# Performance work log

Hardware: AMD Instinct MI355X
Metric: run time of the kernel (lower is better)

## Reference

```python
import jax, jax.numpy as jnp
import numpy as np

N_NODES = 50000
N_EDGES = 800000
IN_FEATS = 256
HEADS = 4
OUT_FEATS = 32
NEG_SLOPE = 0.2


def setup_inputs() -> dict:
    key = jax.random.key(0)
    ks = jax.random.split(key, 8)
    return {
        "feat": jax.random.normal(ks[0], (N_NODES, IN_FEATS), dtype=jnp.float32),
        "edge_weight": jax.random.uniform(ks[1], (N_EDGES,), dtype=jnp.float32),
        "src": jax.random.randint(ks[2], (N_EDGES,), 0, N_NODES, dtype=jnp.int32),
        "dst": jax.random.randint(ks[3], (N_EDGES,), 0, N_NODES, dtype=jnp.int32),
        "W_fc": jax.random.normal(ks[4], (HEADS * OUT_FEATS, IN_FEATS), dtype=jnp.float32) * 0.05,
        "W_edge": jax.random.normal(ks[5], (HEADS * OUT_FEATS, 1), dtype=jnp.float32) * 0.05,
        "attn_l": jax.random.normal(ks[6], (1, HEADS, OUT_FEATS), dtype=jnp.float32) * 0.1,
        "attn_r": jax.random.normal(ks[7], (1, HEADS, OUT_FEATS), dtype=jnp.float32) * 0.1,
        "bias": jnp.zeros((HEADS * OUT_FEATS,), dtype=jnp.float32),
    }


def reference(feat, edge_weight, src, dst, W_fc, W_edge, attn_l, attn_r, bias):
    N = feat.shape[0]
    H, F = attn_l.shape[1], attn_l.shape[2]
    # node projection: [N, H, F]
    feat_hf = (feat @ W_fc.T).reshape(N, H, F)
    el = jnp.sum(feat_hf * attn_l, axis=-1)  # [N, H]
    er = jnp.sum(feat_hf * attn_r, axis=-1)  # [N, H]
    # edgefc(weight.unsqueeze(-1)): Linear(1, H*F) -> weight[e] * W_edge[:,0]
    edge_ft = (edge_weight[:, None] * W_edge[:, 0][None, :]).reshape(-1, H, F)  # [E,H,F]
    # e = leaky_relu(u_add_v(el, er) + edge_ft); broadcast [E,H,1] + [E,H,F]
    e = (el[src] + er[dst])[:, :, None] + edge_ft
    e = jnp.where(e >= 0, e, NEG_SLOPE * e)
    # edge softmax per destination (elementwise over H, F)
    m = jax.ops.segment_max(e, dst, num_segments=N)  # [N,H,F]
    m = jnp.where(jnp.isfinite(m), m, 0.0)
    ex = jnp.exp(e - m[dst])
    s = jax.ops.segment_sum(ex, dst, num_segments=N)  # [N,H,F]
    a = ex / s[dst]
    # weighted aggregation: sum_{e: dst=v} ft[src[e]] * a[e]
    rst = jax.ops.segment_sum(feat_hf[src] * a, dst, num_segments=N)  # [N,H,F]
    rst = rst + bias.reshape(1, H, F)
    return rst
```

## Files before the change

kernel.cpp:

```cpp
#include <hip/hip_runtime.h>

#define NN 50000
#define NE 800000
#define KF 256
#define HF 128
#define NEG 0.2f
#define INVLN2 1.44269504088896340736f

#define NB 391
#define EB 391
#define EPB 2048
#define PREP_BLOCKS 64
#define PROJ_BLOCKS 782

typedef __attribute__((ext_vector_type(8))) short bf16x8;
typedef __attribute__((ext_vector_type(4))) float f32x4;

static __device__ __forceinline__ unsigned bf16_rne(float x) {
  unsigned u = __float_as_uint(x);
  return (u + 0x7fffu + ((u >> 16) & 1u)) >> 16;
}
static __device__ __forceinline__ unsigned cvt_pk(float lo, float hi) {
  unsigned r;
  asm("v_cvt_pk_bf16_f32 %0, %1, %2" : "=v"(r) : "v"(lo), "v"(hi));
  return r;
}
static __device__ __forceinline__ float exp2_raw(float x) {
  float r;
  asm("v_exp_f32 %0, %1" : "=v"(r) : "v"(x));
  return r;
}

__global__ __launch_bounds__(256) void k1_prep_hist(
    const float* __restrict__ Wfc, unsigned* __restrict__ wfcb,
    const int* __restrict__ dst, int* __restrict__ histT) {
  if (blockIdx.x < PREP_BLOCKS) {
    int t = blockIdx.x * 256 + threadIdx.x;
    int e2 = t & 3;
    int l  = (t >> 2) & 63;
    int ct = (t >> 8) & 7;
    int ks = t >> 11;
    int j = ct * 16 + (l & 15);
    int k = ks * 32 + (l >> 4) * 8 + 2 * e2;
    unsigned lo = bf16_rne(Wfc[j * KF + k]);
    unsigned hi = bf16_rne(Wfc[j * KF + k + 1]);
    wfcb[t] = lo | (hi << 16);
    return;
  }
  int e = blockIdx.x - PREP_BLOCKS;
  __shared__ int hist[NB];
  for (int b = threadIdx.x; b < NB; b += 256) hist[b] = 0;
  __syncthreads();
  int base = e * EPB;
  int cnt = min(EPB, NE - base);
  for (int k = threadIdx.x; k < cnt; k += 256) {
    int d = dst[base + k];
    atomicAdd(&hist[d >> 7], 1);
  }
  __syncthreads();
  for (int b = threadIdx.x; b < NB; b += 256) histT[b * EB + e] = hist[b];
}

__global__ __launch_bounds__(256) void k2_proj_scan(
    const float* __restrict__ feat, const unsigned* __restrict__ wfcb,
    unsigned* __restrict__ ftp, const int* __restrict__ histT,
    int* __restrict__ colbase, int* __restrict__ bucketTotal,
    const float* __restrict__ al, const float* __restrict__ ar,
    float* __restrict__ el, float* __restrict__ er) {
  if (blockIdx.x >= PROJ_BLOCKS) {
    int b = blockIdx.x - PROJ_BLOCKS;
    __shared__ int buf[512];
    int t = threadIdx.x;
    int a0 = (t < EB) ? histT[b * EB + t] : 0;
    int a1 = (t + 256 < EB) ? histT[b * EB + t + 256] : 0;
    buf[t] = a0;
    buf[t + 256] = a1;
    __syncthreads();
    for (int o = 1; o < 512; o <<= 1) {
      int x0 = (t >= o) ? buf[t - o] : 0;
      int x1 = buf[t + 256 - o];
      __syncthreads();
      buf[t] += x0;
      buf[t + 256] += x1;
      __syncthreads();
    }
    if (t < EB) colbase[t * NB + b] = buf[t] - a0;
    if (t + 256 < EB) colbase[(t + 256) * NB + b] = buf[t + 256] - a1;
    if (t == 0) bucketTotal[b] = buf[EB - 1];
    return;
  }
  int wid = (blockIdx.x * 256 + threadIdx.x) >> 6;
  if (wid >= NN / 16) return;
  const int lane = threadIdx.x & 63;
  const int m0 = wid * 16;
  const int row = m0 + (lane & 15);
  const int kb = (lane >> 4) * 8;

  f32x4 acc[8];
#pragma unroll
  for (int ct = 0; ct < 8; ct++) acc[ct] = (f32x4){0.f, 0.f, 0.f, 0.f};

  const float4* a4p = (const float4*)(feat + row * KF + kb);
#pragma unroll
  for (int ks = 0; ks < 8; ks++) {
    float4 a0 = a4p[ks * 8];
    float4 a1 = a4p[ks * 8 + 1];
    union { int4 i; bf16x8 s; } ua;
    ua.i = make_int4((int)cvt_pk(a0.x, a0.y), (int)cvt_pk(a0.z, a0.w),
                     (int)cvt_pk(a1.x, a1.y), (int)cvt_pk(a1.z, a1.w));
    bf16x8 af = ua.s;
#pragma unroll
    for (int ct = 0; ct < 8; ct++) {
      union { int4 i; bf16x8 s; } ub;
      ub.i = *(const int4*)&wfcb[((ks * 8 + ct) * 64 + lane) * 4];
      acc[ct] = __builtin_amdgcn_mfma_f32_16x16x32_bf16(af, ub.s, acc[ct], 0, 0, 0);
    }
  }

  const int rbase = m0 + (lane >> 4) * 4;
  const int l15 = lane & 15;
  float alv0[4], alv1[4], arv0[4], arv1[4];
#pragma unroll
  for (int t2 = 0; t2 < 4; t2++) {
    alv0[t2] = al[t2 * 32 + l15];
    alv1[t2] = al[t2 * 32 + 16 + l15];
    arv0[t2] = ar[t2 * 32 + l15];
    arv1[t2] = ar[t2 * 32 + 16 + l15];
  }
  float pl_[4][4], pr_[4][4];
#pragma unroll
  for (int ct2 = 0; ct2 < 4; ct2++) {
#pragma unroll
    for (int r = 0; r < 4; r++) {
      unsigned wv = cvt_pk(acc[2 * ct2][r], acc[2 * ct2 + 1][r]);
      ftp[(rbase + r) * 64 + ct2 * 16 + l15] = wv;
      float f0 = __uint_as_float(wv << 16);
      float f1 = __uint_as_float(wv & 0xffff0000u);
      pl_[r][ct2] = f0 * alv0[ct2] + f1 * alv1[ct2];
      pr_[r][ct2] = f0 * arv0[ct2] + f1 * arv1[ct2];
    }
  }
#pragma unroll
  for (int o = 1; o < 16; o <<= 1) {
#pragma unroll
    for (int r = 0; r < 4; r++) {
#pragma unroll
      for (int hh = 0; hh < 4; hh++) {
        pl_[r][hh] += __shfl_xor(pl_[r][hh], o, 64);
        pr_[r][hh] += __shfl_xor(pr_[r][hh], o, 64);
      }
    }
  }
  if (l15 == 0) {
#pragma unroll
    for (int r = 0; r < 4; r++) {
#pragma unroll
      for (int hh = 0; hh < 4; hh++) {
        el[(rbase + r) * 4 + hh] = pl_[r][hh] * INVLN2;
        er[(rbase + r) * 4 + hh] = pr_[r][hh] * INVLN2;
      }
    }
  }
}

__global__ __launch_bounds__(256) void k4_scatter(
    const int* __restrict__ dst, const int* __restrict__ src,
    const float* __restrict__ ew, const int* __restrict__ colbase,
    const int* __restrict__ bucketTotal, int* __restrict__ bucketBase,
    int2* __restrict__ tmp) {
  __shared__ int buf[512];
  __shared__ int sbase[NB];
  __shared__ int lcnt[NB];
  int t = threadIdx.x;
  int e = blockIdx.x;
  int a0 = (t < NB) ? bucketTotal[t] : 0;
  int a1 = (t + 256 < NB) ? bucketTotal[t + 256] : 0;
  buf[t] = a0;
  buf[t + 256] = a1;
  for (int b = t; b < NB; b += 256) lcnt[b] = 0;
  __syncthreads();
  for (int o = 1; o < 512; o <<= 1) {
    int x0 = (t >= o) ? buf[t - o] : 0;
    int x1 = buf[t + 256 - o];
    __syncthreads();
    buf[t] += x0;
    buf[t + 256] += x1;
    __syncthreads();
  }
  if (t < NB) {
    int bb0 = buf[t] - a0;
    sbase[t] = bb0 + colbase[e * NB + t];
    if (e == 0) bucketBase[t] = bb0;
  }
  if (t + 256 < NB) {
    int bb1 = buf[t + 256] - a1;
    sbase[t + 256] = bb1 + colbase[e * NB + t + 256];
    if (e == 0) bucketBase[t + 256] = bb1;
  }
  if (e == 0 && t == 0) bucketBase[NB] = buf[NB - 1];
  __syncthreads();
  int base = e * EPB;
  int cnt = min(EPB, NE - base);
  for (int k = t; k < cnt; k += 256) {
    int i = base + k;
    int d = dst[i];
    unsigned s = (unsigned)src[i];
    float w = ew[i];
    int r = atomicAdd(&lcnt[d >> 7], 1);
    int pos = sbase[d >> 7] + r;
    tmp[pos] = make_int2((int)(s | ((unsigned)d << 16)), __float_as_int(w));
  }
}

__global__ __launch_bounds__(256) void k5_bucket(
    const int2* __restrict__ tmp, const int* __restrict__ bucketBase,
    int* __restrict__ segbeg, int* __restrict__ segend, int2* __restrict__ es8) {
  int b = blockIdx.x;
  int ebase = bucketBase[b], eend = bucketBase[b + 1];
  int vbase = b * 128;
  __shared__ int cnt[128], buf[128], cur[128];
  int t = threadIdx.x;
  if (t < 128) cnt[t] = 0;
  __syncthreads();
  for (int i = ebase + t; i < eend; i += 256) {
    unsigned x = (unsigned)tmp[i].x;
    atomicAdd(&cnt[(x >> 16) & 127], 1);
  }
  __syncthreads();
  if (t < 128) buf[t] = cnt[t];
  __syncthreads();
  for (int o = 1; o < 128; o <<= 1) {
    int x = (t < 128 && t >= o) ? buf[t - o] : 0;
    __syncthreads();
    if (t < 128) buf[t] += x;
    __syncthreads();
  }
  if (t < 128) {
    cur[t] = buf[t] - cnt[t];
    int v = vbase + t;
    if (v < NN) {
      segbeg[v] = ebase + cur[t];
      segend[v] = ebase + buf[t];
    }
  }
  __syncthreads();
  for (int i = ebase + t; i < eend; i += 256) {
    int2 rec = tmp[i];
    unsigned x = (unsigned)rec.x;
    int r = atomicAdd(&cur[(x >> 16) & 127], 1);
    es8[ebase + r] = make_int2((int)(x & 0xFFFFu), rec.y);
  }
}

__global__ __launch_bounds__(256) void agg_kernel(
    const unsigned* __restrict__ ftp, const float* __restrict__ el,
    const float* __restrict__ er, const int2* __restrict__ es8,
    const int* __restrict__ segbeg, const int* __restrict__ segend,
    const float* __restrict__ We, const float* __restrict__ bias,
    float* __restrict__ out) {
  int wid = (blockIdx.x * blockDim.x + threadIdx.x) >> 6;
  if (wid >= NN) return;
  const int lane = threadIdx.x & 63;
  const int v = wid;
  int beg = __builtin_amdgcn_readfirstlane(segbeg[v]);
  int end = __builtin_amdgcn_readfirstlane(segend[v]);
  const int h = lane >> 4;
  const int c0 = h * 32 + (lane & 15), c1 = c0 + 16;
  const float wx = We[c0] * INVLN2, wy = We[c1] * INVLN2;
  const float bx = bias[c0], by = bias[c1];
  if (beg == end) {
    out[v * HF + c0] = bx;
    out[v * HF + c1] = by;
    return;
  }
  const float erv = er[v * 4 + h];
  float num0 = 0.f, num1 = 0.f, den0 = 0.f, den1 = 0.f;

#define EDGE(w_, u_, e_)                                            \
  {                                                                 \
    float base = (e_) + erv;                                        \
    float t0 = fmaf((w_), wx, base); t0 = fmaxf(t0, NEG * t0);      \
    float t1 = fmaf((w_), wy, base); t1 = fmaxf(t1, NEG * t1);      \
    float x0 = exp2_raw(t0), x1 = exp2_raw(t1);                     \
    float f0 = __uint_as_float((u_) << 16);                         \
    float f1 = __uint_as_float((u_) & 0xffff0000u);                 \
    num0 = fmaf(f0, x0, num0); den0 += x0;                          \
    num1 = fmaf(f1, x1, num1); den1 += x1;                          \
  }

  int i = beg;
  for (; i + 8 <= end; i += 8) {
    int2 q0 = es8[i],     q1 = es8[i + 1], q2 = es8[i + 2], q3 = es8[i + 3];
    int2 q4 = es8[i + 4], q5 = es8[i + 5], q6 = es8[i + 6], q7 = es8[i + 7];
    int s0 = __builtin_amdgcn_readfirstlane(q0.x);
    int s1 = __builtin_amdgcn_readfirstlane(q1.x);
    int s2 = __builtin_amdgcn_readfirstlane(q2.x);
    int s3 = __builtin_amdgcn_readfirstlane(q3.x);
    int s4 = __builtin_amdgcn_readfirstlane(q4.x);
    int s5 = __builtin_amdgcn_readfirstlane(q5.x);
    int s6 = __builtin_amdgcn_readfirstlane(q6.x);
    int s7 = __builtin_amdgcn_readfirstlane(q7.x);
    unsigned u0 = ftp[s0 * 64 + lane], u1 = ftp[s1 * 64 + lane];
    unsigned u2 = ftp[s2 * 64 + lane], u3 = ftp[s3 * 64 + lane];
    unsigned u4 = ftp[s4 * 64 + lane], u5 = ftp[s5 * 64 + lane];
    unsigned u6 = ftp[s6 * 64 + lane], u7 = ftp[s7 * 64 + lane];
    float e0 = el[s0 * 4 + h], e1 = el[s1 * 4 + h];
    float e2 = el[s2 * 4 + h], e3 = el[s3 * 4 + h];
    float e4 = el[s4 * 4 + h], e5 = el[s5 * 4 + h];
    float e6 = el[s6 * 4 + h], e7 = el[s7 * 4 + h];
    float w0 = __uint_as_float(__builtin_amdgcn_readfirstlane(q0.y));
    float w1 = __uint_as_float(__builtin_amdgcn_readfirstlane(q1.y));
    float w2 = __uint_as_float(__builtin_amdgcn_readfirstlane(q2.y));
    float w3 = __uint_as_float(__builtin_amdgcn_readfirstlane(q3.y));
    float w4 = __uint_as_float(__builtin_amdgcn_readfirstlane(q4.y));
    float w5 = __uint_as_float(__builtin_amdgcn_readfirstlane(q5.y));
    float w6 = __uint_as_float(__builtin_amdgcn_readfirstlane(q6.y));
    float w7 = __uint_as_float(__builtin_amdgcn_readfirstlane(q7.y));
    EDGE(w0, u0, e0); EDGE(w1, u1, e1); EDGE(w2, u2, e2); EDGE(w3, u3, e3);
    EDGE(w4, u4, e4); EDGE(w5, u5, e5); EDGE(w6, u6, e6); EDGE(w7, u7, e7);
  }
  for (; i < end; i++) {
    int2 q = es8[i];
    int s = __builtin_amdgcn_readfirstlane(q.x);
    unsigned u = ftp[s * 64 + lane];
    float ee = el[s * 4 + h];
    float w = __uint_as_float(__builtin_amdgcn_readfirstlane(q.y));
    EDGE(w, u, ee);
  }
#undef EDGE

  out[v * HF + c0] = num0 / den0 + bx;
  out[v * HF + c1] = num1 / den1 + by;
}

extern "C" void kernel_launch(void* const* d_in, const int* in_sizes, int n_in,
                              void* d_out, int out_size, void* d_ws, size_t ws_size,
                              hipStream_t stream) {
  const float* feat = (const float*)d_in[0];
  const float* ew   = (const float*)d_in[1];
  const int*   src  = (const int*)d_in[2];
  const int*   dst  = (const int*)d_in[3];
  const float* Wfc  = (const float*)d_in[4];
  const float* We   = (const float*)d_in[5];
  const float* al   = (const float*)d_in[6];
  const float* ar   = (const float*)d_in[7];
  const float* bias = (const float*)d_in[8];
  float* out = (float*)d_out;

  char* ws = (char*)d_ws;
  unsigned* ftp        = (unsigned*)(ws + 0);
  float* el            = (float*)(ws + 12800000);
  float* er            = (float*)(ws + 13600000);
  int* segbeg          = (int*)(ws + 14400000);
  int* segend          = (int*)(ws + 14600000);
  int2* es8            = (int2*)(ws + 14800000);
  int2* tmp            = (int2*)(ws + 21200000);
  int* histT           = (int*)(ws + 27600000);
  int* colbase         = (int*)(ws + 28211524);
  int* bucketTotal     = (int*)(ws + 28823048);
  int* bucketBase      = (int*)(ws + 28824612);
  unsigned* wfcb       = (unsigned*)(ws + 28826180);

  k1_prep_hist<<<PREP_BLOCKS + EB, 256, 0, stream>>>(Wfc, wfcb, dst, histT);
  k2_proj_scan<<<PROJ_BLOCKS + NB, 256, 0, stream>>>(feat, wfcb, ftp, histT, colbase,
                                                     bucketTotal, al, ar, el, er);
  k4_scatter<<<EB, 256, 0, stream>>>(dst, src, ew, colbase, bucketTotal, bucketBase,
                                     tmp);
  k5_bucket<<<NB, 256, 0, stream>>>(tmp, bucketBase, segbeg, segend, es8);
  agg_kernel<<<(NN * 64) / 256, 256, 0, stream>>>(ftp, el, er, es8, segbeg, segend, We,
                                                  bias, out);
}
```

Before: 91.40 us.

## Split node projection across scatter and bucket kernels to overlap latency-bound stages

The MFMA node-projection work is moved out of the scan kernel and split in two halves. Each half is appended as extra blocks to the scatter and bucket-sort kernels. The aim is to let compute-heavy GEMM blocks run alongside the small, atomic-bound histogram and scatter phases, which leave the GPU underused. The scan kernel becomes a standalone lightweight launch. The risk is that the larger proj blocks delay the critical-path scatter blocks, or that register and shared-memory pressure from the fused kernels lowers occupancy.

```diff
diff --git a/kernel.cpp b/kernel.cpp
--- a/kernel.cpp
+++ b/kernel.cpp
@@ -11,7 +11,8 @@
 #define EB 391
 #define EPB 2048
 #define PREP_BLOCKS 64
-#define PROJ_BLOCKS 782
+#define PROJ_WAVES 3125
+#define PH 391
 
 typedef __attribute__((ext_vector_type(8))) short bf16x8;
 typedef __attribute__((ext_vector_type(4))) float f32x4;
@@ -29,6 +30,83 @@
   float r;
   asm("v_exp_f32 %0, %1" : "=v"(r) : "v"(x));
   return r;
+}
+
+static __device__ __forceinline__ void proj_wave(
+    const float* __restrict__ feat, const unsigned* __restrict__ wfcb,
+    unsigned* __restrict__ ftp, const float* __restrict__ al,
+    const float* __restrict__ ar, float* __restrict__ el, float* __restrict__ er,
+    int wid, int lane) {
+  if (wid >= PROJ_WAVES) return;
+  const int m0 = wid * 16;
+  const int row = m0 + (lane & 15);
+  const int kb = (lane >> 4) * 8;
+
+  f32x4 acc[8];
+#pragma unroll
+  for (int ct = 0; ct < 8; ct++) acc[ct] = (f32x4){0.f, 0.f, 0.f, 0.f};
+
+  const float4* a4p = (const float4*)(feat + row * KF + kb);
+#pragma unroll
+  for (int ks = 0; ks < 8; ks++) {
+    float4 a0 = a4p[ks * 8];
+    float4 a1 = a4p[ks * 8 + 1];
+    union { int4 i; bf16x8 s; } ua;
+    ua.i = make_int4((int)cvt_pk(a0.x, a0.y), (int)cvt_pk(a0.z, a0.w),
+                     (int)cvt_pk(a1.x, a1.y), (int)cvt_pk(a1.z, a1.w));
+    bf16x8 af = ua.s;
+#pragma unroll
+    for (int ct = 0; ct < 8; ct++) {
+      union { int4 i; bf16x8 s; } ub;
+      ub.i = *(const int4*)&wfcb[((ks * 8 + ct) * 64 + lane) * 4];
+      acc[ct] = __builtin_amdgcn_mfma_f32_16x16x32_bf16(af, ub.s, acc[ct], 0, 0, 0);
+    }
+  }
+
+  const int rbase = m0 + (lane >> 4) * 4;
+  const int l15 = lane & 15;
+  float alv0[4], alv1[4], arv0[4], arv1[4];
+#pragma unroll
+  for (int t2 = 0; t2 < 4; t2++) {
+    alv0[t2] = al[t2 * 32 + l15];
+    alv1[t2] = al[t2 * 32 + 16 + l15];
+    arv0[t2] = ar[t2 * 32 + l15];
+    arv1[t2] = ar[t2 * 32 + 16 + l15];
+  }
+  float pl_[4][4], pr_[4][4];
+#pragma unroll
+  for (int ct2 = 0; ct2 < 4; ct2++) {
+#pragma unroll
+    for (int r = 0; r < 4; r++) {
+      unsigned wv = cvt_pk(acc[2 * ct2][r], acc[2 * ct2 + 1][r]);
+      ftp[(rbase + r) * 64 + ct2 * 16 + l15] = wv;
+      float f0 = __uint_as_float(wv << 16);
+      float f1 = __uint_as_float(wv & 0xffff0000u);
+      pl_[r][ct2] = f0 * alv0[ct2] + f1 * alv1[ct2];
+      pr_[r][ct2] = f0 * arv0[ct2] + f1 * arv1[ct2];
+    }
+  }
+#pragma unroll
+  for (int o = 1; o < 16; o <<= 1) {
+#pragma unroll
+    for (int r = 0; r < 4; r++) {
+#pragma unroll
+      for (int hh = 0; hh < 4; hh++) {
+        pl_[r][hh] += __shfl_xor(pl_[r][hh], o, 64);
+        pr_[r][hh] += __shfl_xor(pr_[r][hh], o, 64);
+      }
+    }
+  }
+  if (l15 == 0) {
+#pragma unroll
+    for (int r = 0; r < 4; r++) {
+#pragma unroll
+      for (int hh = 0; hh < 4; hh++) {
+        el[(rbase + r) * 4 + hh] = pl_[r][hh] * INVLN2;
+        er[(rbase + r) * 4 + hh] = pr_[r][hh] * INVLN2;
+      }
+    }
+  }
 }
 
 __global__ __launch_bounds__(256) void k1_prep_hist(
@@ -61,113 +139,44 @@
   for (int b = threadIdx.x; b < NB; b += 256) histT[b * EB + e] = hist[b];
 }
 
-__global__ __launch_bounds__(256) void k2_proj_scan(
-    const float* __restrict__ feat, const unsigned* __restrict__ wfcb,
-    unsigned* __restrict__ ftp, const int* __restrict__ histT,
-    int* __restrict__ colbase, int* __restrict__ bucketTotal,
-    const float* __restrict__ al, const float* __restrict__ ar,
-    float* __restrict__ el, float* __restrict__ er) {
-  if (blockIdx.x >= PROJ_BLOCKS) {
-    int b = blockIdx.x - PROJ_BLOCKS;
-    __shared__ int buf[512];
-    int t = threadIdx.x;
-    int a0 = (t < EB) ? histT[b * EB + t] : 0;
-    int a1 = (t + 256 < EB) ? histT[b * EB + t + 256] : 0;
-    buf[t] = a0;
-    buf[t + 256] = a1;
-    __syncthreads();
-    for (int o = 1; o < 512; o <<= 1) {
-      int x0 = (t >= o) ? buf[t - o] : 0;
-      int x1 = buf[t + 256 - o];
-      __syncthreads();
-      buf[t] += x0;
-      buf[t + 256] += x1;
-      __syncthreads();
-    }
-    if (t < EB) colbase[t * NB + b] = buf[t] - a0;
-    if (t + 256 < EB) colbase[(t + 256) * NB + b] = buf[t + 256] - a1;
-    if (t == 0) bucketTotal[b] = buf[EB - 1];
-    return;
-  }
-  int wid = (blockIdx.x * 256 + threadIdx.x) >> 6;
-  if (wid >= NN / 16) return;
-  const int lane = threadIdx.x & 63;
-  const int m0 = wid * 16;
-  const int row = m0 + (lane & 15);
-  const int kb = (lane >> 4) * 8;
-
-  f32x4 acc[8];
-#pragma unroll
-  for (int ct = 0; ct < 8; ct++) acc[ct] = (f32x4){0.f, 0.f, 0.f, 0.f};
-
-  const float4* a4p = (const float4*)(feat + row * KF + kb);
-#pragma unroll
-  for (int ks = 0; ks < 8; ks++) {
-    float4 a0 = a4p[ks * 8];
-    float4 a1 = a4p[ks * 8 + 1];
-    union { int4 i; bf16x8 s; } ua;
-    ua.i = make_int4((int)cvt_pk(a0.x, a0.y), (int)cvt_pk(a0.z, a0.w),
-                     (int)cvt_pk(a1.x, a1.y), (int)cvt_pk(a1.z, a1.w));
-    bf16x8 af = ua.s;
-#pragma unroll
-    for (int ct = 0; ct < 8; ct++) {
-      union { int4 i; bf16x8 s; } ub;
-      ub.i = *(const int4*)&wfcb[((ks * 8 + ct) * 64 + lane) * 4];
-      acc[ct] = __builtin_amdgcn_mfma_f32_16x16x32_bf16(af, ub.s, acc[ct], 0, 0, 0);
-    }
-  }
-
-  const int rbase = m0 + (lane >> 4) * 4;
-  const int l15 = lane & 15;
-  float alv0[4], alv1[4], arv0[4], arv1[4];
-#pragma unroll
-  for (int t2 = 0; t2 < 4; t2++) {
-    alv0[t2] = al[t2 * 32 + l15];
-    alv1[t2] = al[t2 * 32 + 16 + l15];
-    arv0[t2] = ar[t2 * 32 + l15];
-    arv1[t2] = ar[t2 * 32 + 16 + l15];
-  }
-  float pl_[4][4], pr_[4][4];
-#pragma unroll
-  for (int ct2 = 0; ct2 < 4; ct2++) {
-#pragma unroll
-    for (int r = 0; r < 4; r++) {
-      unsigned wv = cvt_pk(acc[2 * ct2][r], acc[2 * ct2 + 1][r]);
-      ftp[(rbase + r) * 64 + ct2 * 16 + l15] = wv;
-      float f0 = __uint_as_float(wv << 16);
-      float f1 = __uint_as_float(wv & 0xffff0000u);
-      pl_[r][ct2] = f0 * alv0[ct2] + f1 * alv1[ct2];
-      pr_[r][ct2] = f0 * arv0[ct2] + f1 * arv1[ct2];
-    }
-  }
-#pragma unroll
-  for (int o = 1; o < 16; o <<= 1) {
-#pragma unroll
-    for (int r = 0; r < 4; r++) {
-#pragma unroll
-      for (int hh = 0; hh < 4; hh++) {
-        pl_[r][hh] += __shfl_xor(pl_[r][hh], o, 64);
-        pr_[r][hh] += __shfl_xor(pr_[r][hh], o, 64);
-      }
-    }
-  }
-  if (l15 == 0) {
-#pragma unroll
-    for (int r = 0; r < 4; r++) {
-#pragma unroll
-      for (int hh = 0; hh < 4; hh++) {
-        el[(rbase + r) * 4 + hh] = pl_[r][hh] * INVLN2;
-        er[(rbase + r) * 4 + hh] = pr_[r][hh] * INVLN2;
-      }
-    }
-  }
-}
-
-__global__ __launch_bounds__(256) void k4_scatter(
+__global__ __launch_bounds__(256) void k2_scan(
+    const int* __restrict__ histT, int* __restrict__ colbase,
+    int* __restrict__ bucketTotal) {
+  int b = blockIdx.x;
+  __shared__ int buf[512];
+  int t = threadIdx.x;
+  int a0 = (t < EB) ? histT[b * EB + t] : 0;
+  int a1 = (t + 256 < EB) ? histT[b * EB + t + 256] : 0;
+  buf[t] = a0;
+  buf[t + 256] = a1;
+  __syncthreads();
+  for (int o = 1; o < 512; o <<= 1) {
+    int x0 = (t >= o) ? buf[t - o] : 0;
+    int x1 = buf[t + 256 - o];
+    __syncthreads();
+    buf[t] += x0;
+    buf[t + 256] += x1;
+    __syncthreads();
+  }
+  if (t < EB) colbase[t * NB + b] = buf[t] - a0;
+  if (t + 256 < EB) colbase[(t + 256) * NB + b] = buf[t + 256] - a1;
+  if (t == 0) bucketTotal[b] = buf[EB - 1];
+}
+
+__global__ __launch_bounds__(256) void k4_scatter_proj(
     const int* __restrict__ dst, const int* __restrict__ src,
     const float* __restrict__ ew, const int* __restrict__ colbase,
     const int* __restrict__ bucketTotal, int* __restrict__ bucketBase,
-    int2* __restrict__ tmp) {
+    int2* __restrict__ tmp,
+    const float* __restrict__ feat, const unsigned* __restrict__ wfcb,
+    unsigned* __restrict__ ftp, const float* __restrict__ al,
+    const float* __restrict__ ar, float* __restrict__ el, float* __restrict__ er) {
+  if (blockIdx.x >= EB) {
+    int pidx = blockIdx.x - EB;
+    proj_wave(feat, wfcb, ftp, al, ar, el, er,
+              (pidx * 256 + (int)threadIdx.x) >> 6, threadIdx.x & 63);
+    return;
+  }
   __shared__ int buf[512];
   __shared__ int sbase[NB];
   __shared__ int lcnt[NB];
@@ -212,9 +221,18 @@
   }
 }
 
-__global__ __launch_bounds__(256) void k5_bucket(
+__global__ __launch_bounds__(256) void k5_bucket_proj(
     const int2* __restrict__ tmp, const int* __restrict__ bucketBase,
-    int* __restrict__ segbeg, int* __restrict__ segend, int2* __restrict__ es8) {
+    int* __restrict__ segbeg, int* __restrict__ segend, int2* __restrict__ es8,
+    const float* __restrict__ feat, const unsigned* __restrict__ wfcb,
+    unsigned* __restrict__ ftp, const float* __restrict__ al,
+    const float* __restrict__ ar, float* __restrict__ el, float* __restrict__ er) {
+  if (blockIdx.x >= NB) {
+    int pidx = (blockIdx.x - NB) + PH;
+    proj_wave(feat, wfcb, ftp, al, ar, el, er,
+              (pidx * 256 + (int)threadIdx.x) >> 6, threadIdx.x & 63);
+    return;
+  }
   int b = blockIdx.x;
   int ebase = bucketBase[b], eend = bucketBase[b + 1];
   int vbase = b * 128;
@@ -362,11 +380,12 @@
   unsigned* wfcb       = (unsigned*)(ws + 28826180);
 
   k1_prep_hist<<<PREP_BLOCKS + EB, 256, 0, stream>>>(Wfc, wfcb, dst, histT);
-  k2_proj_scan<<<PROJ_BLOCKS + NB, 256, 0, stream>>>(feat, wfcb, ftp, histT, colbase,
-                                                     bucketTotal, al, ar, el, er);
-  k4_scatter<<<EB, 256, 0, stream>>>(dst, src, ew, colbase, bucketTotal, bucketBase,
-                                     tmp);
-  k5_bucket<<<NB, 256, 0, stream>>>(tmp, bucketBase, segbeg, segend, es8);
+  k2_scan<<<NB, 256, 0, stream>>>(histT, colbase, bucketTotal);
+  k4_scatter_proj<<<EB + PH, 256, 0, stream>>>(dst, src, ew, colbase, bucketTotal,
+                                               bucketBase, tmp, feat, wfcb, ftp, al,
+                                               ar, el, er);
+  k5_bucket_proj<<<NB + PH, 256, 0, stream>>>(tmp, bucketBase, segbeg, segend, es8,
+                                              feat, wfcb, ftp, al, ar, el, er);
   agg_kernel<<<(NN * 64) / 256, 256, 0, stream>>>(ftp, el, er, es8, segbeg, segend, We,
                                                   bias, out);
 }
```

Measured after the change: 90.06 us. Within noise of the previous version (-1.5%).
